# Kernel optimization log

Measured on AMD Instinct MI355X. Metric: run time of the kernel, lower is better.

## Reference

```python
import jax, jax.numpy as jnp
import numpy as np

TAU = 0.8
ALPHA = 0.1
N_CLASSES = 100


def _normalize(x, axis=-1, eps=1e-12):
    # Matches torch.nn.functional.normalize (L2, eps clamp)
    return x / jnp.maximum(jnp.linalg.norm(x, axis=axis, keepdims=True), eps)


def setup_inputs() -> dict:
    key = jax.random.key(0)
    k1, k2, k3, k4 = jax.random.split(key, 4)
    bs, C, H, W = 32, 512, 14, 14
    m_sz = 16384
    queries = jax.random.normal(k1, (bs, C, H, W), dtype=jnp.float32)
    targets = jax.random.randint(k2, (bs,), 0, N_CLASSES)
    m_keys = _normalize(jax.random.normal(k3, (m_sz, C), dtype=jnp.float32))
    m_vals = jax.random.randint(k4, (m_sz,), 0, N_CLASSES).astype(jnp.int32)
    return {"queries": queries, "targets": targets, "m_keys": m_keys, "m_vals": m_vals}


def reference(queries, targets, m_keys, m_vals):
    # Eval-mode forward of Memory (upd_memory/use_centroid side effects excluded):
    # per-sample key similarity matmul + top-1 retrieval + masked triplet margin loss,
    # fully batched instead of the original python loop over the batch.
    bs, C, H, W = queries.shape
    n_hw = H * W
    q = queries.reshape(bs, C, n_hw).transpose(0, 2, 1)      # [bs, n_hw, C]
    q = _normalize(q, axis=-1)
    sims = jnp.einsum('bnc,mc->bnm', q, m_keys)               # [bs, n_hw, m_sz]

    # nearest memory slot per spatial location, then majority vote over locations
    nearest_val = m_vals[jnp.argmax(sims, axis=-1)]           # [bs, n_hw]
    counts = jnp.sum(nearest_val[:, :, None] == jnp.arange(N_CLASSES)[None, None, :],
                     axis=1)                                   # [bs, N_CLASSES]
    fetched_vals = jnp.argmax(counts, axis=-1).astype(jnp.int32)

    # masked pos/neg nearest similarities (mask by multiply, as in the original)
    correct = (m_vals[None, :] == targets[:, None])           # [bs, m_sz]
    pos = jnp.max(sims * correct[:, None, :], axis=-1)        # [bs, n_hw]
    neg = jnp.max(sims * (~correct)[:, None, :], axis=-1)     # [bs, n_hw]
    has_pos = jnp.any(correct, axis=-1)                       # [bs]
    per_loc = jnp.where(has_pos[:, None],
                        jax.nn.relu(neg - pos + ALPHA),
                        jax.nn.relu(neg + ALPHA))
    memory_loss = jnp.sum(jnp.mean(per_loc, axis=-1))         # sum over batch of per-sample means
    return fetched_vals, memory_loss
```

## Files before the change

### kernel.cpp

```cpp
#include <hip/hip_runtime.h>
#include <hip/hip_bf16.h>
#include <math.h>

typedef __attribute__((ext_vector_type(8))) short short8b;
typedef __attribute__((ext_vector_type(4))) float f32x4;

#define BSZ 32
#define NHW 196
#define M_ROWS 6272
#define MPAD 6400
#define CDIM 512
#define MSZ 16384
#define NCLS 100
#define ALPHA 0.1f

__global__ __launch_bounds__(256) void k_invnorm4(const float* __restrict__ q,
                                                  float* __restrict__ ssq4,
                                                  int* __restrict__ gcount) {
    int b = blockIdx.x, cc = blockIdx.y, n = threadIdx.x;
    if (b == 0 && cc == 0) { gcount[n] = 0; gcount[256 + n] = 0; }
    if (n >= NHW) return;
    const float* base = q + ((size_t)b * CDIM + cc * 128) * NHW + n;
    float ss = 0.f;
#pragma unroll 8
    for (int c = 0; c < 128; ++c) { float v = base[(size_t)c * NHW]; ss = fmaf(v, v, ss); }
    ssq4[(size_t)(b * NHW + n) * 4 + cc] = ss;
}

__global__ __launch_bounds__(256) void k_decomp_q(
    const float* __restrict__ Q, const float* __restrict__ ssq4,
    unsigned short* __restrict__ qhi, float* __restrict__ qn)
{
    __shared__ unsigned short lh[32][65];
    __shared__ float fs[32][65];
    const int t = threadIdx.x;
    const int rb = blockIdx.x % 100, kb = blockIdx.x / 100;
    const int r0 = rb * 64, c0 = kb * 32;
    const int cin = t >> 6, rin = t & 63;
    const int r = r0 + rin;
    float iv = 0.f;
    if (r < M_ROWS) {
        const float4 s4 = *reinterpret_cast<const float4*>(ssq4 + (size_t)r * 4);
        iv = 1.f / fmaxf(sqrtf((s4.x + s4.y) + (s4.z + s4.w)), 1e-12f);
    }
    const int b = r / NHW, n = r - b * NHW;
#pragma unroll
    for (int ci = 0; ci < 8; ++ci) {
        int cl = ci * 4 + cin;
        float x = 0.f;
        if (r < M_ROWS) x = Q[((size_t)(b * CDIM + (c0 + cl))) * NHW + n] * iv;
        __hip_bfloat16 h = __float2bfloat16(x);
        lh[cl][rin] = *(unsigned short*)&h;
        fs[cl][rin] = x;
    }
    __syncthreads();
    const int r2 = t >> 2, seg = t & 3;
    short8b vh;
    float4 f0, f1;
#pragma unroll
    for (int i = 0; i < 8; ++i) vh[i] = (short)lh[seg * 8 + i][r2];
    f0.x = fs[seg * 8 + 0][r2]; f0.y = fs[seg * 8 + 1][r2];
    f0.z = fs[seg * 8 + 2][r2]; f0.w = fs[seg * 8 + 3][r2];
    f1.x = fs[seg * 8 + 4][r2]; f1.y = fs[seg * 8 + 5][r2];
    f1.z = fs[seg * 8 + 6][r2]; f1.w = fs[seg * 8 + 7][r2];
    size_t off = ((size_t)kb * MPAD + r0 + r2) * 32 + seg * 8;
    *(short8b*)(qhi + off) = vh;
    float* qb = qn + (size_t)(r0 + r2) * CDIM + c0 + seg * 8;
    *reinterpret_cast<float4*>(qb) = f0;
    *reinterpret_cast<float4*>(qb + 4) = f1;
}

__global__ __launch_bounds__(256) void k_decomp_k(
    const float* __restrict__ K, unsigned short* __restrict__ khi)
{
    int tid = blockIdx.x * 256 + threadIdx.x;
    int c4 = tid & 127, key = tid >> 7;
    int c = c4 << 2;
    const float4 v = *reinterpret_cast<const float4*>(K + (size_t)key * CDIM + c);
    float xs[4] = {v.x, v.y, v.z, v.w};
    unsigned short hs[4];
#pragma unroll
    for (int i = 0; i < 4; ++i) {
        __hip_bfloat16 h = __float2bfloat16(xs[i]);
        hs[i] = *(unsigned short*)&h;
    }
    size_t off = ((size_t)(c >> 5) * MSZ + key) * 32 + (c & 31);
    ushort4 H; H.x = hs[0]; H.y = hs[1]; H.z = hs[2]; H.w = hs[3];
    *reinterpret_cast<ushort4*>(khi + off) = H;
}

__device__ __forceinline__ void gload16(const void* g, void* lds) {
    __builtin_amdgcn_global_load_lds((const __attribute__((address_space(1))) void*)g,
                                     (__attribute__((address_space(3))) void*)lds,
                                     16, 0, 0);
}

__global__ __launch_bounds__(256, 3) void k_mfma(
    const unsigned short* __restrict__ qhi, const unsigned short* __restrict__ khi,
    const int* __restrict__ mvals, const int* __restrict__ tgt,
    float* __restrict__ pmax32, float* __restrict__ ppos, float* __restrict__ pneg)
{
    __shared__ char smem[32768];
    __shared__ int mv_s[128];

    const int tid = threadIdx.x;
    const int w = tid >> 6, l = tid & 63;

    const int xcd = blockIdx.x & 7;
    const int idx = blockIdx.x >> 3;
    const int mt = idx >> 4;
    const int nt = (xcd << 4) | (idx & 15);
    const int r0 = mt * 128, n0 = nt * 128;

    const int srow = l >> 2;
    const int sg8 = (((l & 3) ^ ((l >> 3) & 3)) << 3);
    const int fr = l & 15;
    const int abyte = (fr << 6) + ((((l >> 4) ^ ((l >> 1) & 3))) << 4);

    const int wm = w >> 1, wn = w & 1;
    const int arow0 = wm * 64, bcol0 = wn * 64;

    f32x4 acc[4][4];
    const f32x4 zero4 = {0.f, 0.f, 0.f, 0.f};
#pragma unroll
    for (int m = 0; m < 4; ++m)
#pragma unroll
        for (int n = 0; n < 4; ++n) acc[m][n] = zero4;

    if (tid < 128) mv_s[tid] = mvals[n0 + tid];

    for (int ks = 0; ks < 8; ++ks) {
        __syncthreads();
#pragma unroll
        for (int h = 0; h < 2; ++h) {
            const int kb = 2 * ks + h;
            const size_t qb = ((size_t)kb * MPAD + r0) * 32;
            const size_t ko = ((size_t)kb * MSZ + n0) * 32;
#pragma unroll
            for (int j = 0; j < 2; ++j) {
                const int rr = w * 32 + j * 16 + srow;
                const int dst = h * 8192 + w * 2048 + j * 1024;
                gload16(qhi + qb + (size_t)rr * 32 + sg8, smem + dst);
                gload16(khi + ko + (size_t)rr * 32 + sg8, smem + 16384 + dst);
            }
        }
        __syncthreads();
#pragma unroll
        for (int h = 0; h < 2; ++h) {
            const char* bq = smem + h * 8192;
            const char* bk = smem + 16384 + h * 8192;
            short8b bh[4], ah[4];
#pragma unroll
            for (int n = 0; n < 4; ++n)
                bh[n] = *(const short8b*)(bk + ((bcol0 + n * 16) << 6) + abyte);
#pragma unroll
            for (int m = 0; m < 4; ++m)
                ah[m] = *(const short8b*)(bq + ((arow0 + m * 16) << 6) + abyte);
#pragma unroll
            for (int m = 0; m < 4; ++m)
#pragma unroll
                for (int n = 0; n < 4; ++n)
                    acc[m][n] = __builtin_amdgcn_mfma_f32_16x16x32_bf16(ah[m], bh[n], acc[m][n], 0, 0, 0);
        }
    }
    __syncthreads();

#pragma unroll
    for (int m = 0; m < 4; ++m) {
#pragma unroll
        for (int rg = 0; rg < 4; ++rg) {
            const int rloc = arow0 + m * 16 + ((l >> 4) << 2) + rg;
            const int rglob = r0 + rloc;
            int samp = rglob / NHW; samp = samp > 31 ? 31 : samp;
            const int tg = tgt[samp];
            float p = -INFINITY, ng = -INFINITY;
            float vh0 = -INFINITY, vh1 = -INFINITY;
#pragma unroll
            for (int n = 0; n < 4; ++n) {
                const int cl = bcol0 + n * 16 + fr;
                const float v = acc[m][n][rg];
                const bool corr = (mv_s[cl] == tg);
                p  = fmaxf(p,  corr ? v : 0.f);
                ng = fmaxf(ng, corr ? 0.f : v);
                if (n < 2) vh0 = fmaxf(vh0, v); else vh1 = fmaxf(vh1, v);
            }
#pragma unroll
            for (int off = 1; off < 16; off <<= 1) {
                p   = fmaxf(p,   __shfl_xor(p,   off, 16));
                ng  = fmaxf(ng,  __shfl_xor(ng,  off, 16));
                vh0 = fmaxf(vh0, __shfl_xor(vh0, off, 16));
                vh1 = fmaxf(vh1, __shfl_xor(vh1, off, 16));
            }
            if (fr == 0) {
                ppos[(size_t)(nt * 2 + wn) * MPAD + rglob] = p;
                pneg[(size_t)(nt * 2 + wn) * MPAD + rglob] = ng;
                pmax32[(size_t)rglob * 512 + nt * 4 + wn * 2 + 0] = vh0;
                pmax32[(size_t)rglob * 512 + nt * 4 + wn * 2 + 1] = vh1;
            }
        }
    }
}

__global__ __launch_bounds__(256) void k_plan(
    const float* __restrict__ pmax32,
    int* __restrict__ gcount, unsigned short* __restrict__ gtasks,
    unsigned long long* __restrict__ packed)
{
    __shared__ float redm[4];
    const int row = blockIdx.x, t = threadIdx.x;
    const float m0 = pmax32[(size_t)row * 512 + t];
    const float m1 = pmax32[(size_t)row * 512 + 256 + t];
    float m = fmaxf(m0, m1);
#pragma unroll
    for (int off = 1; off < 64; off <<= 1) m = fmaxf(m, __shfl_xor(m, off));
    if ((t & 63) == 0) redm[t >> 6] = m;
    __syncthreads();
    const float M = fmaxf(fmaxf(redm[0], redm[1]), fmaxf(redm[2], redm[3]));
    const float thr = M - 0.010f;
    if (t == 0) packed[row] = 0ull;
    if (m0 >= thr) {
        int s = atomicAdd(&gcount[t], 1);
        gtasks[(size_t)t * M_ROWS + s] = (unsigned short)row;
    }
    if (m1 >= thr) {
        int s = atomicAdd(&gcount[256 + t], 1);
        gtasks[(size_t)(256 + t) * M_ROWS + s] = (unsigned short)row;
    }
}

__device__ __forceinline__ unsigned long long enc_vi(float v, int idx) {
    unsigned u = __float_as_uint(v);
    u = (u & 0x80000000u) ? ~u : (u | 0x80000000u);
    return ((unsigned long long)u << 32) | (unsigned)(0xFFFFFFFFu - (unsigned)idx);
}

__global__ __launch_bounds__(256, 2) void k_redot(
    const float* __restrict__ qn, const float* __restrict__ mk,
    const int* __restrict__ gcount, const unsigned short* __restrict__ gtasks,
    unsigned long long* __restrict__ packed)
{
    __shared__ float ks[32][516];
    __shared__ float qrow[512];
    __shared__ float part[32][9];
    const int g = blockIdx.x, t = threadIdx.x;
    const int cnt = gcount[g];
    if (cnt == 0) return;
    {
        const float4* src = reinterpret_cast<const float4*>(mk + (size_t)g * 32 * CDIM);
        for (int i = t; i < 4096; i += 256) {
            const int key = i >> 7, pos = i & 127;
            *reinterpret_cast<float4*>(&ks[key][pos << 2]) = src[i];
        }
    }
    const int kj = t & 31, seg = t >> 5;
    for (int i = 0; i < cnt; ++i) {
        const int row = gtasks[(size_t)g * M_ROWS + i];
        *reinterpret_cast<float2*>(&qrow[t * 2]) =
            *reinterpret_cast<const float2*>(qn + (size_t)row * CDIM + t * 2);
        __syncthreads();
        float s = 0.f;
        const float4* kr = reinterpret_cast<const float4*>(&ks[kj][seg * 64]);
        const float4* qr = reinterpret_cast<const float4*>(&qrow[seg * 64]);
#pragma unroll
        for (int u = 0; u < 16; ++u) {
            const float4 a = qr[u], b = kr[u];
            s = fmaf(a.x, b.x, s); s = fmaf(a.y, b.y, s);
            s = fmaf(a.z, b.z, s); s = fmaf(a.w, b.w, s);
        }
        part[kj][seg] = s;
        __syncthreads();
        if (t < 32) {
            float sim = ((part[t][0] + part[t][1]) + (part[t][2] + part[t][3]))
                      + ((part[t][4] + part[t][5]) + (part[t][6] + part[t][7]));
            int ki = g * 32 + t;
#pragma unroll
            for (int off = 1; off < 32; off <<= 1) {
                const float ov = __shfl_xor(sim, off);
                const int   oi = __shfl_xor(ki, off);
                if (ov > sim || (ov == sim && oi < ki)) { sim = ov; ki = oi; }
            }
            if (t == 0)
                atomicMax((unsigned long long*)&packed[row], enc_vi(sim, ki));
        }
        __syncthreads();
    }
}

__global__ __launch_bounds__(256) void k_merge(
    const int* __restrict__ mvals, const int* __restrict__ tgt,
    const unsigned long long* __restrict__ packed,
    const float* __restrict__ ppos, const float* __restrict__ pneg,
    float* __restrict__ out, float* __restrict__ means)
{
    __shared__ int counts[NCLS];
    __shared__ float perloc[256];
    __shared__ int haspos;
    const int b = blockIdx.x, t = threadIdx.x;
    if (t == 0) haspos = 0;
    if (t < NCLS) counts[t] = 0;
    perloc[t] = 0.f;
    __syncthreads();
    const int tg = tgt[b];
    int found = 0;
    for (int i = t; i < MSZ; i += 256) found |= (mvals[i] == tg) ? 1 : 0;
    if (found) atomicOr(&haspos, 1);
    __syncthreads();
    if (t < NHW) {
        const int row = b * NHW + t;
        float p = -INFINITY, ng = -INFINITY;
        for (int c = 0; c < 256; ++c) {
            p  = fmaxf(p,  ppos[(size_t)c * MPAD + row]);
            ng = fmaxf(ng, pneg[(size_t)c * MPAD + row]);
        }
        const int ri = (int)(0xFFFFFFFFu - (unsigned)(packed[row] & 0xFFFFFFFFull));
        atomicAdd(&counts[mvals[ri]], 1);
        perloc[t] = haspos ? fmaxf(ng - p + ALPHA, 0.f)
                           : fmaxf(ng + ALPHA, 0.f);
    }
    __syncthreads();
    for (int s = 128; s > 0; s >>= 1) {
        if (t < s) perloc[t] += perloc[t + s];
        __syncthreads();
    }
    if (t == 0) {
        int bestc = 0, bestn = counts[0];
        for (int c = 1; c < NCLS; ++c)
            if (counts[c] > bestn) { bestn = counts[c]; bestc = c; }
        out[b] = (float)bestc;
        means[b] = perloc[0] / (float)NHW;
    }
}

__global__ __launch_bounds__(64) void k_final(const float* __restrict__ means,
                                              float* __restrict__ out) {
    if (threadIdx.x == 0) {
        float s = 0.f;
        for (int b = 0; b < BSZ; ++b) s += means[b];
        out[BSZ] = s;
    }
}

#define BM 128
#define BN 128
#define BK 16
#define LDA (BM + 4)
#define LDB (BN + 4)

__global__ __launch_bounds__(256) void k_invnorm(const float* __restrict__ q,
                                                 float* __restrict__ invq) {
    int b = blockIdx.x, n = threadIdx.x;
    if (n >= NHW) return;
    const float* base = q + (size_t)b * CDIM * NHW + n;
    float ss = 0.f;
#pragma unroll 4
    for (int c = 0; c < CDIM; ++c) { float v = base[(size_t)c * NHW]; ss = fmaf(v, v, ss); }
    invq[b * NHW + n] = 1.f / fmaxf(sqrtf(ss), 1e-12f);
}

__global__ __launch_bounds__(256) void k_gemm_reduce(
    const float* __restrict__ Q, const float* __restrict__ Kz,
    const int* __restrict__ mvals, const int* __restrict__ tgt,
    const float* __restrict__ invq,
    float* __restrict__ pmax, int* __restrict__ pidx,
    float* __restrict__ ppos, float* __restrict__ pneg)
{
    __shared__ float As[BK][LDA];
    __shared__ float Bs[BK][LDB];
    __shared__ float run_max[BM];
    __shared__ int   run_idx[BM];
    __shared__ float run_pos[BM];
    __shared__ float run_neg[BM];
    __shared__ int   mv_s[BN];
    __shared__ int   tgt_s[BM];
    __shared__ float inv_s[BM];

    const int t = threadIdx.x;
    const int rt = blockIdx.x % 49;
    const int chunk = blockIdx.x / 49;
    const int r0 = rt * BM;

    if (t < BM) {
        run_max[t] = -INFINITY; run_idx[t] = 0;
        run_pos[t] = -INFINITY; run_neg[t] = -INFINITY;
        int row = r0 + t;
        tgt_s[t] = tgt[row / NHW];
        inv_s[t] = invq[row];
    }
    const int ty = t >> 4, tx = t & 15;
    __syncthreads();

    for (int tile = 0; tile < 8; ++tile) {
        const int key0 = chunk * 1024 + tile * BN;
        if (t < BN) mv_s[t] = mvals[key0 + t];
        float acc[8][8];
#pragma unroll
        for (int i = 0; i < 8; ++i)
#pragma unroll
            for (int j = 0; j < 8; ++j) acc[i][j] = 0.f;

        for (int ks = 0; ks < 32; ++ks) {
            const int c0 = ks * BK;
            __syncthreads();
#pragma unroll
            for (int it = 0; it < 2; ++it) {
                int i = t + it * 256;
                int k = i >> 5;
                int r4 = (i & 31) << 2;
                int row = r0 + r4;
                int b = row / NHW;
                int n = row - b * NHW;
                const float4 v = *reinterpret_cast<const float4*>(
                    Q + ((size_t)(b * CDIM + c0 + k)) * NHW + n);
                float4 w;
                w.x = v.x * inv_s[r4 + 0]; w.y = v.y * inv_s[r4 + 1];
                w.z = v.z * inv_s[r4 + 2]; w.w = v.w * inv_s[r4 + 3];
                *reinterpret_cast<float4*>(&As[k][r4]) = w;
            }
#pragma unroll
            for (int it = 0; it < 2; ++it) {
                int i = t + it * 256;
                int key = i >> 2;
                int cc = (i & 3) << 2;
                const float4 v = *reinterpret_cast<const float4*>(
                    Kz + (size_t)(key0 + key) * CDIM + c0 + cc);
                Bs[cc + 0][key] = v.x; Bs[cc + 1][key] = v.y;
                Bs[cc + 2][key] = v.z; Bs[cc + 3][key] = v.w;
            }
            __syncthreads();
#pragma unroll
            for (int k = 0; k < BK; ++k) {
                float4 a0 = *reinterpret_cast<const float4*>(&As[k][4 * ty]);
                float4 a1 = *reinterpret_cast<const float4*>(&As[k][64 + 4 * ty]);
                float4 b0 = *reinterpret_cast<const float4*>(&Bs[k][4 * tx]);
                float4 b1 = *reinterpret_cast<const float4*>(&Bs[k][64 + 4 * tx]);
                float a[8] = {a0.x, a0.y, a0.z, a0.w, a1.x, a1.y, a1.z, a1.w};
                float bb[8] = {b0.x, b0.y, b0.z, b0.w, b1.x, b1.y, b1.z, b1.w};
#pragma unroll
                for (int i = 0; i < 8; ++i)
#pragma unroll
                    for (int j = 0; j < 8; ++j)
                        acc[i][j] = fmaf(a[i], bb[j], acc[i][j]);
            }
        }
#pragma unroll
        for (int i = 0; i < 8; ++i) {
            int rl = (i < 4) ? (4 * ty + i) : (64 + 4 * ty + i - 4);
            int tgti = tgt_s[rl];
            float vmax = -INFINITY; int vidx = 0;
            float p = -INFINITY, ng = -INFINITY;
#pragma unroll
            for (int j = 0; j < 8; ++j) {
                int cl = (j < 4) ? (4 * tx + j) : (64 + 4 * tx + j - 4);
                float v = acc[i][j];
                int gk = key0 + cl;
                if (v > vmax) { vmax = v; vidx = gk; }
                bool corr = (mv_s[cl] == tgti);
                p  = fmaxf(p,  corr ? v : 0.f);
                ng = fmaxf(ng, corr ? 0.f : v);
            }
#pragma unroll
            for (int off = 1; off < 16; off <<= 1) {
                float om = __shfl_xor(vmax, off, 16);
                int   oi = __shfl_xor(vidx, off, 16);
                float op = __shfl_xor(p,    off, 16);
                float on = __shfl_xor(ng,   off, 16);
                if (om > vmax || (om == vmax && oi < vidx)) { vmax = om; vidx = oi; }
                p = fmaxf(p, op); ng = fmaxf(ng, on);
            }
            if (tx == 0) {
                if (vmax > run_max[rl]) { run_max[rl] = vmax; run_idx[rl] = vidx; }
                run_pos[rl] = fmaxf(run_pos[rl], p);
                run_neg[rl] = fmaxf(run_neg[rl], ng);
            }
        }
        __syncthreads();
    }
    if (t < BM) {
        int row = r0 + t;
        size_t o = (size_t)row * 16 + chunk;
        pmax[o] = run_max[t]; pidx[o] = run_idx[t];
        ppos[o] = run_pos[t]; pneg[o] = run_neg[t];
    }
}

__global__ __launch_bounds__(256) void k_merge_fb(
    const int* __restrict__ mvals, const int* __restrict__ tgt,
    const float* __restrict__ pmax, const int* __restrict__ pidx,
    const float* __restrict__ ppos, const float* __restrict__ pneg,
    float* __restrict__ out, float* __restrict__ means, int nch)
{
    __shared__ int counts[NCLS];
    __shared__ float perloc[256];
    __shared__ int haspos;
    const int b = blockIdx.x, t = threadIdx.x;
    if (t == 0) haspos = 0;
    if (t < NCLS) counts[t] = 0;
    perloc[t] = 0.f;
    __syncthreads();
    const int tg = tgt[b];
    int found = 0;
    for (int i = t; i < MSZ; i += 256) found |= (mvals[i] == tg) ? 1 : 0;
    if (found) atomicOr(&haspos, 1);
    __syncthreads();
    if (t < NHW) {
        int row = b * NHW + t;
        float vmax = -INFINITY; int vidx = 0;
        float p = -INFINITY, ng = -INFINITY;
        for (int c = 0; c < nch; ++c) {
            size_t o = (size_t)row * nch + c;
            float m = pmax[o]; int i_ = pidx[o];
            if (m > vmax || (m == vmax && i_ < vidx)) { vmax = m; vidx = i_; }
            p = fmaxf(p, ppos[o]); ng = fmaxf(ng, pneg[o]);
        }
        atomicAdd(&counts[mvals[vidx]], 1);
        perloc[t] = haspos ? fmaxf(ng - p + ALPHA, 0.f)
                           : fmaxf(ng + ALPHA, 0.f);
    }
    __syncthreads();
    for (int s = 128; s > 0; s >>= 1) {
        if (t < s) perloc[t] += perloc[t + s];
        __syncthreads();
    }
    if (t == 0) {
        int bestc = 0, bestn = counts[0];
        for (int c = 1; c < NCLS; ++c)
            if (counts[c] > bestn) { bestn = counts[c]; bestc = c; }
        out[b] = (float)bestc;
        means[b] = perloc[0] / (float)NHW;
    }
}

extern "C" void kernel_launch(void* const* d_in, const int* in_sizes, int n_in,
                              void* d_out, int out_size, void* d_ws, size_t ws_size,
                              hipStream_t stream) {
    const float* q  = (const float*)d_in[0];
    const int*   tg = (const int*)d_in[1];
    const float* mk = (const float*)d_in[2];
    const int*   mv = (const int*)d_in[3];
    float* out = (float*)d_out;

    unsigned short* khi = (unsigned short*)d_ws;
    unsigned short* qhi = khi + (size_t)MSZ * CDIM;
    float* qn     = (float*)(qhi + (size_t)MPAD * CDIM);
    float* ssq4   = qn + (size_t)MPAD * CDIM;
    float* pmax32 = ssq4 + (size_t)M_ROWS * 4;
    float* ppos   = pmax32 + (size_t)MPAD * 512;
    float* pneg   = ppos + (size_t)MPAD * 256;
    int*   gcount = (int*)(pneg + (size_t)MPAD * 256);
    unsigned short* gtasks = (unsigned short*)(gcount + 512);
    unsigned long long* packed = (unsigned long long*)(gtasks + (size_t)512 * M_ROWS);
    float* means  = (float*)(packed + M_ROWS);
    size_t need = (size_t)((char*)(means + BSZ) - (char*)d_ws);

    if (ws_size >= need) {
        k_invnorm4<<<dim3(BSZ, 4), 256, 0, stream>>>(q, ssq4, gcount);
        k_decomp_q<<<1600, 256, 0, stream>>>(q, ssq4, qhi, qn);
        k_decomp_k<<<(MSZ * 128) / 256, 256, 0, stream>>>(mk, khi);
        k_mfma<<<6400, 256, 0, stream>>>(qhi, khi, mv, tg, pmax32, ppos, pneg);
        k_plan<<<M_ROWS, 256, 0, stream>>>(pmax32, gcount, gtasks, packed);
        k_redot<<<512, 256, 0, stream>>>(qn, mk, gcount, gtasks, packed);
        k_merge<<<BSZ, 256, 0, stream>>>(mv, tg, packed, ppos, pneg, out, means);
        k_final<<<1, 64, 0, stream>>>(means, out);
    } else {
        float* invq0  = (float*)d_ws;
        float* pmax0  = invq0 + M_ROWS;
        float* ppos0  = pmax0 + (size_t)M_ROWS * 16;
        float* pneg0  = ppos0 + (size_t)M_ROWS * 16;
        int*   pidx0  = (int*)(pneg0 + (size_t)M_ROWS * 16);
        float* means0 = (float*)(pidx0 + (size_t)M_ROWS * 16);
        k_invnorm<<<BSZ, 256, 0, stream>>>(q, invq0);
        k_gemm_reduce<<<49 * 16, 256, 0, stream>>>(q, mk, mv, tg, invq0,
                                                   pmax0, pidx0, ppos0, pneg0);
        k_merge_fb<<<BSZ, 256, 0, stream>>>(mv, tg, pmax0, pidx0, ppos0, pneg0, out, means0, 16);
        k_final<<<1, 64, 0, stream>>>(means0, out);
    }
}
```

Baseline: 304.4 us.

## Replace shuffle reductions in MFMA epilogue with LDS row reductions

The MFMA kernel epilogue now writes per-lane partial pos/neg and half-tile maxima into a padded shared-memory buffer and reduces them across both column-waves, instead of doing 16-lane xor-shuffle reductions per row. This halves the ppos/pneg partial buffers (one per column tile instead of per wave), so the merge kernel scans 128 partials instead of 256. Per-row target lookups are hoisted by precomputing correctness masks for the at most two samples a tile spans. The LDS buffer grows to about 34KB while launch bounds ask for 4 blocks per CU. The extra barriers could cost occupancy or latency.

```diff
diff --git a/kernel.cpp b/kernel.cpp
--- a/kernel.cpp
+++ b/kernel.cpp
@@ -13,6 +13,7 @@
 #define MSZ 16384
 #define NCLS 100
 #define ALPHA 0.1f
+#define RSTR 67
 
 __global__ __launch_bounds__(256) void k_invnorm4(const float* __restrict__ q,
                                                   float* __restrict__ ssq4,
@@ -95,13 +96,14 @@
                                      16, 0, 0);
 }
 
-__global__ __launch_bounds__(256, 3) void k_mfma(
+__global__ __launch_bounds__(256, 4) void k_mfma(
     const unsigned short* __restrict__ qhi, const unsigned short* __restrict__ khi,
     const int* __restrict__ mvals, const int* __restrict__ tgt,
     float* __restrict__ pmax32, float* __restrict__ ppos, float* __restrict__ pneg)
 {
-    __shared__ char smem[32768];
+    __shared__ __align__(16) float red[128 * RSTR];
     __shared__ int mv_s[128];
+    char* smem = (char*)red;
 
     const int tid = threadIdx.x;
     const int w = tid >> 6, l = tid & 63;
@@ -165,6 +167,17 @@
     }
     __syncthreads();
 
+    const int s0 = r0 / NHW;
+    int s1 = (r0 + 127) / NHW; if (s1 > 31) s1 = 31;
+    const int tg0 = tgt[s0], tg1 = tgt[s1];
+    bool c0m[4], c1m[4];
+#pragma unroll
+    for (int n = 0; n < 4; ++n) {
+        const int cl = bcol0 + n * 16 + fr;
+        c0m[n] = (mv_s[cl] == tg0);
+        c1m[n] = (mv_s[cl] == tg1);
+    }
+
 #pragma unroll
     for (int m = 0; m < 4; ++m) {
 #pragma unroll
@@ -172,32 +185,52 @@
             const int rloc = arow0 + m * 16 + ((l >> 4) << 2) + rg;
             const int rglob = r0 + rloc;
             int samp = rglob / NHW; samp = samp > 31 ? 31 : samp;
-            const int tg = tgt[samp];
+            const bool use0 = (samp == s0);
             float p = -INFINITY, ng = -INFINITY;
-            float vh0 = -INFINITY, vh1 = -INFINITY;
 #pragma unroll
             for (int n = 0; n < 4; ++n) {
-                const int cl = bcol0 + n * 16 + fr;
                 const float v = acc[m][n][rg];
-                const bool corr = (mv_s[cl] == tg);
+                const bool corr = use0 ? c0m[n] : c1m[n];
                 p  = fmaxf(p,  corr ? v : 0.f);
                 ng = fmaxf(ng, corr ? 0.f : v);
-                if (n < 2) vh0 = fmaxf(vh0, v); else vh1 = fmaxf(vh1, v);
-            }
-#pragma unroll
-            for (int off = 1; off < 16; off <<= 1) {
-                p   = fmaxf(p,   __shfl_xor(p,   off, 16));
-                ng  = fmaxf(ng,  __shfl_xor(ng,  off, 16));
-                vh0 = fmaxf(vh0, __shfl_xor(vh0, off, 16));
-                vh1 = fmaxf(vh1, __shfl_xor(vh1, off, 16));
-            }
-            if (fr == 0) {
-                ppos[(size_t)(nt * 2 + wn) * MPAD + rglob] = p;
-                pneg[(size_t)(nt * 2 + wn) * MPAD + rglob] = ng;
-                pmax32[(size_t)rglob * 512 + nt * 4 + wn * 2 + 0] = vh0;
-                pmax32[(size_t)rglob * 512 + nt * 4 + wn * 2 + 1] = vh1;
-            }
-        }
+            }
+            red[rloc * RSTR + (wn << 4) + fr] = p;
+            red[rloc * RSTR + 34 + (wn << 4) + fr] = ng;
+        }
+    }
+    __syncthreads();
+    {
+        const int row = tid & 127;
+        const int base = row * RSTR + ((tid < 128) ? 0 : 34);
+        float v = red[base];
+#pragma unroll 31
+        for (int i = 1; i < 32; ++i) v = fmaxf(v, red[base + i]);
+        if (tid < 128) ppos[(size_t)nt * MPAD + r0 + row] = v;
+        else           pneg[(size_t)nt * MPAD + r0 + row] = v;
+    }
+    __syncthreads();
+
+#pragma unroll
+    for (int m = 0; m < 4; ++m) {
+#pragma unroll
+        for (int rg = 0; rg < 4; ++rg) {
+            const int rloc = arow0 + m * 16 + ((l >> 4) << 2) + rg;
+            const float vh0 = fmaxf(acc[m][0][rg], acc[m][1][rg]);
+            const float vh1 = fmaxf(acc[m][2][rg], acc[m][3][rg]);
+            red[rloc * RSTR + (wn << 5) + fr] = vh0;
+            red[rloc * RSTR + (wn << 5) + 16 + fr] = vh1;
+        }
+    }
+    __syncthreads();
+#pragma unroll
+    for (int uu = 0; uu < 2; ++uu) {
+        const int u = tid + uu * 256;
+        const int row = u >> 2, grp = u & 3;
+        const int base = row * RSTR + (grp << 4);
+        float v = red[base];
+#pragma unroll 15
+        for (int i = 1; i < 16; ++i) v = fmaxf(v, red[base + i]);
+        pmax32[(size_t)(r0 + row) * 512 + (nt << 2) + grp] = v;
     }
 }
 
@@ -308,7 +341,7 @@
     if (t < NHW) {
         const int row = b * NHW + t;
         float p = -INFINITY, ng = -INFINITY;
-        for (int c = 0; c < 256; ++c) {
+        for (int c = 0; c < 128; ++c) {
             p  = fmaxf(p,  ppos[(size_t)c * MPAD + row]);
             ng = fmaxf(ng, pneg[(size_t)c * MPAD + row]);
         }
@@ -545,8 +578,8 @@
     float* ssq4   = qn + (size_t)MPAD * CDIM;
     float* pmax32 = ssq4 + (size_t)M_ROWS * 4;
     float* ppos   = pmax32 + (size_t)MPAD * 512;
-    float* pneg   = ppos + (size_t)MPAD * 256;
-    int*   gcount = (int*)(pneg + (size_t)MPAD * 256);
+    float* pneg   = ppos + (size_t)MPAD * 128;
+    int*   gcount = (int*)(pneg + (size_t)MPAD * 128);
     unsigned short* gtasks = (unsigned short*)(gcount + 512);
     unsigned long long* packed = (unsigned long long*)(gtasks + (size_t)512 * M_ROWS);
     float* means  = (float*)(packed + M_ROWS);
```

Result: faster. 248.1 us (-18.5%).
